# Performance work log

Measured on AMD Instinct MI355X. Metric: run time of the kernel, lower is better.

The kernel has to match this reference:

```python
import jax, jax.numpy as jnp
import numpy as np

B, T, D, H = 64, 1024, 1024, 1024


def setup_inputs() -> dict:
    key = jax.random.key(0)
    k = jax.random.split(key, 5)
    s = 1.0 / np.sqrt(H)  # torch RNNCell init: U(-1/sqrt(H), 1/sqrt(H))
    return {
        "x": jax.random.normal(k[0], (B, T, D), jnp.float32),
        "W_ih": jax.random.uniform(k[1], (H, D), jnp.float32, -s, s),
        "W_hh": jax.random.uniform(k[2], (H, H), jnp.float32, -s, s),
        "b_ih": jax.random.uniform(k[3], (H,), jnp.float32, -s, s),
        "b_hh": jax.random.uniform(k[4], (H,), jnp.float32, -s, s),
    }


def reference(x, W_ih, W_hh, b_ih, b_hh):
    # DelayLineRNN2xOS with a tanh RNNCell:
    #   for i in range(T//2):
    #     h_eve = cell(x[:, 2i],   h_eve); states[:, 2i]   = h_eve
    #     h_odd = cell(x[:, 2i-1], h_odd); states[:, 2i-1] = h_odd   (note 2*0-1 == -1)
    Bn, Tn, _ = x.shape
    Hn = W_hh.shape[0]
    half = Tn // 2

    idx_eve = jnp.arange(half) * 2          # 0, 2, ..., T-2
    idx_odd = (idx_eve - 1) % Tn            # T-1, 1, 3, ..., T-3  (Python neg-index at i=0)

    # Precompute input projections for all timesteps (both biases folded in).
    gi = jnp.einsum('btd,hd->bth', x, W_ih) + b_ih + b_hh  # [B, T, H]
    ge = gi[:, idx_eve].transpose(1, 0, 2)                  # [half, B, H]
    go = gi[:, idx_odd].transpose(1, 0, 2)                  # [half, B, H]

    h0 = jnp.zeros((Bn, Hn), x.dtype)

    def step(carry, inp):
        he, ho = carry
        a, b = inp
        he = jnp.tanh(a + he @ W_hh.T)
        ho = jnp.tanh(b + ho @ W_hh.T)
        return (he, ho), (he, ho)

    (he_f, ho_f), (eve_s, odd_s) = jax.lax.scan(step, (h0, h0), (ge, go))

    # eve_s[i] -> slot 2i ; odd_s[i] -> slot (2i-1) mod T, i.e. sorted odd slots
    # [1, 3, ..., T-1] receive odd_s rolled left by one.
    odd_sorted = jnp.roll(odd_s, -1, axis=0)                # [half, B, H]
    states = jnp.stack([eve_s, odd_sorted], axis=1)         # [half, 2, B, H]
    states = states.reshape(Tn, Bn, Hn).transpose(1, 0, 2)  # [B, T, H]

    return states, he_f[None]  # (states, h_final[1, B, H])
```

## Files before the change

### kernel.cpp

```cpp
#include <hip/hip_runtime.h>

#define B_    64
#define T_    1024
#define H_    1024
#define HALF_ 512
#define NWG_SCAN 128
#define HBUF_HALF 131072

typedef short bf16x8 __attribute__((ext_vector_type(8)));
typedef short bf16x4 __attribute__((ext_vector_type(4)));
typedef _Float16 f16x8 __attribute__((ext_vector_type(8)));
typedef float f32x4  __attribute__((ext_vector_type(4)));
typedef unsigned int u32x4 __attribute__((ext_vector_type(4)));

__device__ __forceinline__ short f2bf(float f) {
    unsigned u = __builtin_bit_cast(unsigned, f);
    u += 0x7fffu + ((u >> 16) & 1u);
    return (short)(u >> 16);
}

__device__ __forceinline__ short f2h(float f) {
    return (short)__builtin_bit_cast(unsigned short, (_Float16)f);
}

__device__ __forceinline__ float tanh_fast(float x) {
    return 1.0f - 2.0f / (__expf(2.0f * x) + 1.0f);
}

__global__ __launch_bounds__(256) void gi_gemm(
        const float* __restrict__ X, const float* __restrict__ Wih,
        const float* __restrict__ bih, const float* __restrict__ bhh,
        float* __restrict__ out) {
    __shared__ short As[128][40];
    __shared__ short Bs[128][40];
    const int bid = blockIdx.x;
    const int tn = bid & 7;
    const int tm = bid >> 3;
    const int tid = threadIdx.x;
    const int l  = tid & 63;
    const int w  = tid >> 6;
    const int wr = w >> 1, wc = w & 1;
    const int lc = l & 15,  lr = l >> 4;

    const float* Ab = X   + (size_t)tm * 128 * 1024;
    const float* Bb = Wih + (size_t)tn * 128 * 1024;
    const int srow = tid >> 3;
    const int sc4  = (tid & 7) * 4;

    f32x4 acc[4][4];
#pragma unroll
    for (int m = 0; m < 4; m++)
#pragma unroll
        for (int n = 0; n < 4; n++) acc[m][n] = (f32x4){0.f, 0.f, 0.f, 0.f};

    f32x4 ra[4], rb[4];
#pragma unroll
    for (int c = 0; c < 4; c++) {
        ra[c] = *reinterpret_cast<const f32x4*>(Ab + (size_t)(srow + 32*c) * 1024 + sc4);
        rb[c] = *reinterpret_cast<const f32x4*>(Bb + (size_t)(srow + 32*c) * 1024 + sc4);
    }

    for (int k0 = 0; k0 < 1024; k0 += 32) {
        __syncthreads();
#pragma unroll
        for (int c = 0; c < 4; c++) {
            bf16x4 va = { f2bf(ra[c].x), f2bf(ra[c].y), f2bf(ra[c].z), f2bf(ra[c].w) };
            bf16x4 vb = { f2bf(rb[c].x), f2bf(rb[c].y), f2bf(rb[c].z), f2bf(rb[c].w) };
            *reinterpret_cast<bf16x4*>(&As[srow + 32*c][sc4]) = va;
            *reinterpret_cast<bf16x4*>(&Bs[srow + 32*c][sc4]) = vb;
        }
        __syncthreads();
        if (k0 + 32 < 1024) {
            const float* Ak = Ab + k0 + 32;
            const float* Bk = Bb + k0 + 32;
#pragma unroll
            for (int c = 0; c < 4; c++) {
                ra[c] = *reinterpret_cast<const f32x4*>(Ak + (size_t)(srow + 32*c) * 1024 + sc4);
                rb[c] = *reinterpret_cast<const f32x4*>(Bk + (size_t)(srow + 32*c) * 1024 + sc4);
            }
        }
        bf16x8 af[4], bfr[4];
#pragma unroll
        for (int m = 0; m < 4; m++)
            af[m] = *reinterpret_cast<bf16x8*>(&As[wr*64 + m*16 + lc][lr*8]);
#pragma unroll
        for (int n = 0; n < 4; n++)
            bfr[n] = *reinterpret_cast<bf16x8*>(&Bs[wc*64 + n*16 + lc][lr*8]);
#pragma unroll
        for (int m = 0; m < 4; m++)
#pragma unroll
            for (int n = 0; n < 4; n++)
                acc[m][n] = __builtin_amdgcn_mfma_f32_16x16x32_bf16(af[m], bfr[n], acc[m][n], 0, 0, 0);
    }

#pragma unroll
    for (int n = 0; n < 4; n++) {
        const int col = tn*128 + wc*64 + n*16 + lc;
        const float bs = bih[col] + bhh[col];
#pragma unroll
        for (int m = 0; m < 4; m++) {
            const int row0 = tm*128 + wr*64 + m*16 + lr*4;
#pragma unroll
            for (int j = 0; j < 4; j++)
                out[(size_t)(row0 + j) * 1024 + col] = acc[m][n][j] + bs;
        }
    }
}

__global__ __launch_bounds__(256, 1) void rnn_scan(
        const float* __restrict__ Whh, float* __restrict__ out,
        short* __restrict__ hbuf) {
    __shared__ short hB[16 * 1024];
    __shared__ short htr[16 * 68];
    const int wg = blockIdx.x;
    const int p  = wg >> 6;
    const int g  = (wg >> 4) & 3;
    const int s  = wg & 15;
    const int tid = threadIdx.x;
    const int l  = tid & 63;
    const int w  = tid >> 6;
    const int lc = l & 15, lr = l >> 4;
    const int sb = tid >> 4;
    const int sg = tid & 15;

    bf16x8 breg[32];
    {
        const float* wrow = Whh + (size_t)(s*64 + w*16 + lc) * 1024;
#pragma unroll
        for (int kc = 0; kc < 32; kc++) {
            f32x4 v0 = *reinterpret_cast<const f32x4*>(wrow + kc*32 + lr*8);
            f32x4 v1 = *reinterpret_cast<const f32x4*>(wrow + kc*32 + lr*8 + 4);
            bf16x8 q = { f2h(v0.x), f2h(v0.y), f2h(v0.z), f2h(v0.w),
                         f2h(v1.x), f2h(v1.y), f2h(v1.z), f2h(v1.w) };
            breg[kc] = q;
        }
    }

    const unsigned hload_base = (unsigned)((p*64 + g*16 + sb) * 1024 + sg*8);
    const unsigned hstore_off = (unsigned)((p*64 + g*16 + sb) * 1024 + s*64 + sg*4);
    const int col = s*64 + w*16 + lc;

    for (int step = 0; step < HALF_; step++) {
        const int tt = (p == 0) ? (2*step) : (step == 0 ? T_-1 : 2*step - 1);
        const int epw = step % 3 + 1;
        const int epv = (step + 2) % 3 + 1;
        f32x4 acc = (f32x4){0.f, 0.f, 0.f, 0.f};
        float gi[4]; unsigned ob[4];

        if (step) {
            bf16x8 hl[8];
            const short* hc = hbuf + (size_t)((step+1) & 1) * HBUF_HALF + hload_base;
#pragma unroll
            for (int c = 0; c < 8; c++)
                asm volatile("global_load_dwordx4 %0, %1, off sc0 sc1"
                             : "=v"(hl[c]) : "v"(hc + c*128) : "memory");
#pragma unroll
            for (int j = 0; j < 4; j++) {
                ob[j] = (unsigned)(((g*16 + lr*4 + j) * T_ + tt) * H_ + col);
                gi[j] = out[ob[j]];
            }
            const unsigned pat = (unsigned)((epv & 1) | (((epv >> 1) & 1) << 16));
            unsigned pend = 0;
            asm volatile("s_waitcnt vmcnt(4)" ::: "memory");
            __builtin_amdgcn_sched_barrier(0);
#pragma unroll
            for (int c = 0; c < 8; c++) {
                u32x4 d = __builtin_bit_cast(u32x4, hl[c]);
                unsigned m = ((d[0] & 0x00010001u) ^ pat) | ((d[1] & 0x00010001u) ^ pat)
                           | ((d[2] & 0x00010001u) ^ pat) | ((d[3] & 0x00010001u) ^ pat);
                if (!__all(m == 0)) pend |= 1u << c;
            }
            while (pend) {
#pragma unroll
                for (int c = 0; c < 8; c++)
                    if (pend & (1u << c))
                        asm volatile("global_load_dwordx4 %0, %1, off sc0 sc1"
                                     : "=v"(hl[c]) : "v"(hc + c*128) : "memory");
                asm volatile("s_waitcnt vmcnt(0)" ::: "memory");
                __builtin_amdgcn_sched_barrier(0);
#pragma unroll
                for (int c = 0; c < 8; c++) {
                    if (pend & (1u << c)) {
                        u32x4 d = __builtin_bit_cast(u32x4, hl[c]);
                        unsigned m = ((d[0] & 0x00010001u) ^ pat) | ((d[1] & 0x00010001u) ^ pat)
                                   | ((d[2] & 0x00010001u) ^ pat) | ((d[3] & 0x00010001u) ^ pat);
                        if (__all(m == 0)) pend &= ~(1u << c);
                    }
                }
            }
#pragma unroll
            for (int c = 0; c < 8; c++) {
                bf16x4 lo = { hl[c][0], hl[c][1], hl[c][2], hl[c][3] };
                bf16x4 hi = { hl[c][4], hl[c][5], hl[c][6], hl[c][7] };
                const int g8 = (sg + c*16) * 2;
                *reinterpret_cast<bf16x4*>(&hB[sb*1024 + (((g8    ) ^ sb) << 2)]) = lo;
                *reinterpret_cast<bf16x4*>(&hB[sb*1024 + (((g8 + 1) ^ sb) << 2)]) = hi;
            }
            __syncthreads();
            f32x4 a0 = (f32x4){0,0,0,0}, a1 = (f32x4){0,0,0,0};
            f32x4 a2 = (f32x4){0,0,0,0}, a3 = (f32x4){0,0,0,0};
#pragma unroll
            for (int kc = 0; kc < 32; kc += 4) {
#pragma unroll
                for (int q = 0; q < 4; q++) {
                    const int k8 = (kc + q) * 8 + lr * 2;
                    bf16x4 lo = *reinterpret_cast<const bf16x4*>(&hB[lc*1024 + (((k8    ) ^ lc) << 2)]);
                    bf16x4 hi = *reinterpret_cast<const bf16x4*>(&hB[lc*1024 + (((k8 + 1) ^ lc) << 2)]);
                    bf16x8 hf = { lo[0], lo[1], lo[2], lo[3], hi[0], hi[1], hi[2], hi[3] };
                    f32x4& aq = (q == 0) ? a0 : (q == 1) ? a1 : (q == 2) ? a2 : a3;
                    aq = __builtin_amdgcn_mfma_f32_16x16x32_f16(
                        __builtin_bit_cast(f16x8, hf),
                        __builtin_bit_cast(f16x8, breg[kc + q]), aq, 0, 0, 0);
                }
            }
            acc = (a0 + a1) + (a2 + a3);
        } else {
#pragma unroll
            for (int j = 0; j < 4; j++) {
                ob[j] = (unsigned)(((g*16 + lr*4 + j) * T_ + tt) * H_ + col);
                gi[j] = out[ob[j]];
            }
        }

        const unsigned short ebit = (unsigned short)((lc & 1) ? ((epw >> 1) & 1) : (epw & 1));
        float hv[4];
#pragma unroll
        for (int j = 0; j < 4; j++) {
            hv[j] = tanh_fast(acc[j] + gi[j]);
            unsigned short u = __builtin_bit_cast(unsigned short, (_Float16)hv[j]);
            u = (unsigned short)((u & 0xFFFEu) | ebit);
            htr[(lr*4 + j)*68 + w*16 + lc] = (short)u;
        }
        __syncthreads();

        if (step < HALF_ - 1) {
            bf16x4 v = *reinterpret_cast<bf16x4*>(&htr[sb*68 + sg*4]);
            short* hn = hbuf + (size_t)(step & 1) * HBUF_HALF + hstore_off;
            asm volatile("global_store_dwordx2 %0, %1, off sc0 sc1"
                         :: "v"(hn), "v"(v) : "memory");
        }

#pragma unroll
        for (int j = 0; j < 4; j++) {
            out[ob[j]] = hv[j];
            if (p == 0 && step == HALF_ - 1)
                out[(unsigned)(B_*T_*H_) + (unsigned)((g*16 + lr*4 + j) * H_ + col)] = hv[j];
        }
    }
}

extern "C" void kernel_launch(void* const* d_in, const int* in_sizes, int n_in,
                              void* d_out, int out_size, void* d_ws, size_t ws_size,
                              hipStream_t stream) {
    const float* X   = (const float*)d_in[0];
    const float* Wih = (const float*)d_in[1];
    const float* Whh = (const float*)d_in[2];
    const float* bih = (const float*)d_in[3];
    const float* bhh = (const float*)d_in[4];
    float* out = (float*)d_out;

    short* hbuf = (short*)d_ws;

    hipMemsetAsync(hbuf, 0, (size_t)2 * HBUF_HALF * 2, stream);
    gi_gemm<<<dim3(4096), dim3(256), 0, stream>>>(X, Wih, bih, bhh, out);
    rnn_scan<<<dim3(NWG_SCAN), dim3(256), 0, stream>>>(Whh, out, hbuf);
}
```

Before: 2.094 ms.

## Remap scan workgroups per XCD and poll hidden state through local L2

New measurement: 4.353 ms. 2.08x slower.

```diff
diff --git a/kernel.cpp b/kernel.cpp
--- a/kernel.cpp
+++ b/kernel.cpp
@@ -6,6 +6,7 @@
 #define HALF_ 512
 #define NWG_SCAN 128
 #define HBUF_HALF 131072
+#define LOCAL_ROUNDS 8
 
 typedef short bf16x8 __attribute__((ext_vector_type(8)));
 typedef short bf16x4 __attribute__((ext_vector_type(4)));
@@ -109,13 +110,13 @@
 
 __global__ __launch_bounds__(256, 1) void rnn_scan(
         const float* __restrict__ Whh, float* __restrict__ out,
-        short* __restrict__ hbuf) {
+        short* __restrict__ hloc, short* __restrict__ hrem) {
     __shared__ short hB[16 * 1024];
     __shared__ short htr[16 * 68];
     const int wg = blockIdx.x;
-    const int p  = wg >> 6;
-    const int g  = (wg >> 4) & 3;
-    const int s  = wg & 15;
+    const int p  = (wg >> 2) & 1;
+    const int g  = wg & 3;
+    const int s  = wg >> 3;
     const int tid = threadIdx.x;
     const int l  = tid & 63;
     const int w  = tid >> 6;
@@ -149,11 +150,13 @@
 
         if (step) {
             bf16x8 hl[8];
-            const short* hc = hbuf + (size_t)((step+1) & 1) * HBUF_HALF + hload_base;
+            const size_t hoff = (size_t)((step+1) & 1) * HBUF_HALF + hload_base;
+            const short* hcl = hloc + hoff;
+            const short* hcr = hrem + hoff;
 #pragma unroll
             for (int c = 0; c < 8; c++)
-                asm volatile("global_load_dwordx4 %0, %1, off sc0 sc1"
-                             : "=v"(hl[c]) : "v"(hc + c*128) : "memory");
+                asm volatile("global_load_dwordx4 %0, %1, off sc0"
+                             : "=v"(hl[c]) : "v"(hcl + c*128) : "memory");
 #pragma unroll
             for (int j = 0; j < 4; j++) {
                 ob[j] = (unsigned)(((g*16 + lr*4 + j) * T_ + tt) * H_ + col);
@@ -170,12 +173,21 @@
                            | ((d[2] & 0x00010001u) ^ pat) | ((d[3] & 0x00010001u) ^ pat);
                 if (!__all(m == 0)) pend |= 1u << c;
             }
+            int rounds = 0;
             while (pend) {
-#pragma unroll
-                for (int c = 0; c < 8; c++)
-                    if (pend & (1u << c))
-                        asm volatile("global_load_dwordx4 %0, %1, off sc0 sc1"
-                                     : "=v"(hl[c]) : "v"(hc + c*128) : "memory");
+                if (rounds < LOCAL_ROUNDS) {
+#pragma unroll
+                    for (int c = 0; c < 8; c++)
+                        if (pend & (1u << c))
+                            asm volatile("global_load_dwordx4 %0, %1, off sc0"
+                                         : "=v"(hl[c]) : "v"(hcl + c*128) : "memory");
+                } else {
+#pragma unroll
+                    for (int c = 0; c < 8; c++)
+                        if (pend & (1u << c))
+                            asm volatile("global_load_dwordx4 %0, %1, off sc0 sc1"
+                                         : "=v"(hl[c]) : "v"(hcr + c*128) : "memory");
+                }
                 asm volatile("s_waitcnt vmcnt(0)" ::: "memory");
                 __builtin_amdgcn_sched_barrier(0);
 #pragma unroll
@@ -187,6 +199,7 @@
                         if (__all(m == 0)) pend &= ~(1u << c);
                     }
                 }
+                rounds++;
             }
 #pragma unroll
             for (int c = 0; c < 8; c++) {
@@ -235,9 +248,13 @@
 
         if (step < HALF_ - 1) {
             bf16x4 v = *reinterpret_cast<bf16x4*>(&htr[sb*68 + sg*4]);
-            short* hn = hbuf + (size_t)(step & 1) * HBUF_HALF + hstore_off;
+            const size_t off = (size_t)(step & 1) * HBUF_HALF + hstore_off;
+            short* hnl = hloc + off;
+            short* hnr = hrem + off;
+            asm volatile("global_store_dwordx2 %0, %1, off sc0"
+                         :: "v"(hnl), "v"(v) : "memory");
             asm volatile("global_store_dwordx2 %0, %1, off sc0 sc1"
-                         :: "v"(hn), "v"(v) : "memory");
+                         :: "v"(hnr), "v"(v) : "memory");
         }
 
 #pragma unroll
@@ -259,9 +276,10 @@
     const float* bhh = (const float*)d_in[4];
     float* out = (float*)d_out;
 
-    short* hbuf = (short*)d_ws;
-
-    hipMemsetAsync(hbuf, 0, (size_t)2 * HBUF_HALF * 2, stream);
+    short* hloc = (short*)d_ws;
+    short* hrem = hloc + 2 * HBUF_HALF;
+
+    hipMemsetAsync(d_ws, 0, (size_t)2 * HBUF_HALF * 2 * 2, stream);
     gi_gemm<<<dim3(4096), dim3(256), 0, stream>>>(X, Wih, bih, bhh, out);
-    rnn_scan<<<dim3(NWG_SCAN), dim3(256), 0, stream>>>(Whh, out, hbuf);
-}
+    rnn_scan<<<dim3(NWG_SCAN), dim3(256), 0, stream>>>(Whh, out, hloc, hrem);
+}
```

## Software-pipeline next-step h and gi loads in RNN scan, vectorize output stores

Applied to the files above, without the earlier changes.

After: 2.287 ms. +9.2%, slower.

```diff
diff --git a/kernel.cpp b/kernel.cpp
--- a/kernel.cpp
+++ b/kernel.cpp
@@ -26,6 +26,14 @@
 __device__ __forceinline__ float tanh_fast(float x) {
     return 1.0f - 2.0f / (__expf(2.0f * x) + 1.0f);
 }
+
+#define BAR() do { \
+    __builtin_amdgcn_sched_barrier(0); \
+    asm volatile("s_waitcnt lgkmcnt(0)" ::: "memory"); \
+    __builtin_amdgcn_sched_barrier(0); \
+    __builtin_amdgcn_s_barrier(); \
+    __builtin_amdgcn_sched_barrier(0); \
+} while (0)
 
 __global__ __launch_bounds__(256) void gi_gemm(
         const float* __restrict__ X, const float* __restrict__ Wih,
@@ -107,11 +115,126 @@
     }
 }
 
+#define STEP_BODY(STEP_, GIC_, GIN_)                                           \
+{                                                                              \
+    const int step = (STEP_);                                                  \
+    const int epw = step % 3 + 1;                                              \
+    const int epv = (step + 2) % 3 + 1;                                        \
+    f32x4 acc;                                                                 \
+    if (step) {                                                                \
+        asm volatile("s_waitcnt vmcnt(2)" ::: "memory");                       \
+        __builtin_amdgcn_sched_barrier(0);                                     \
+        const unsigned pat = (unsigned)((epv & 1) | (((epv >> 1) & 1) << 16)); \
+        unsigned pend = 0;                                                     \
+        _Pragma("unroll")                                                      \
+        for (int c = 0; c < 8; c++) {                                          \
+            u32x4 d = __builtin_bit_cast(u32x4, hl[c]);                        \
+            unsigned m = ((d[0] & 0x00010001u) ^ pat) | ((d[1] & 0x00010001u) ^ pat)  \
+                       | ((d[2] & 0x00010001u) ^ pat) | ((d[3] & 0x00010001u) ^ pat); \
+            if (!__all(m == 0)) pend |= 1u << c;                               \
+        }                                                                      \
+        const short* hc = hbuf + (size_t)((step+1) & 1) * HBUF_HALF + hload_base; \
+        while (pend) {                                                         \
+            _Pragma("unroll")                                                  \
+            for (int c = 0; c < 8; c++)                                        \
+                if (pend & (1u << c))                                          \
+                    asm volatile("global_load_dwordx4 %0, %1, off sc0 sc1"     \
+                                 : "=v"(hl[c]) : "v"(hc + c*128) : "memory");  \
+            asm volatile("s_waitcnt vmcnt(0)" ::: "memory");                   \
+            __builtin_amdgcn_sched_barrier(0);                                 \
+            _Pragma("unroll")                                                  \
+            for (int c = 0; c < 8; c++) {                                      \
+                if (pend & (1u << c)) {                                        \
+                    u32x4 d = __builtin_bit_cast(u32x4, hl[c]);                \
+                    unsigned m = ((d[0] & 0x00010001u) ^ pat) | ((d[1] & 0x00010001u) ^ pat)  \
+                               | ((d[2] & 0x00010001u) ^ pat) | ((d[3] & 0x00010001u) ^ pat); \
+                    if (__all(m == 0)) pend &= ~(1u << c);                     \
+                }                                                              \
+            }                                                                  \
+        }                                                                      \
+        _Pragma("unroll")                                                      \
+        for (int c = 0; c < 8; c++) {                                          \
+            bf16x4 lo = { hl[c][0], hl[c][1], hl[c][2], hl[c][3] };            \
+            bf16x4 hi = { hl[c][4], hl[c][5], hl[c][6], hl[c][7] };            \
+            const int g8 = (sg + c*16) * 2;                                    \
+            *reinterpret_cast<bf16x4*>(&hB[sb*1024 + (((g8    ) ^ sb) << 2)]) = lo; \
+            *reinterpret_cast<bf16x4*>(&hB[sb*1024 + (((g8 + 1) ^ sb) << 2)]) = hi; \
+        }                                                                      \
+        BAR();                                                                 \
+        f32x4 a0 = (f32x4){0,0,0,0}, a1 = (f32x4){0,0,0,0};                    \
+        f32x4 a2 = (f32x4){0,0,0,0}, a3 = (f32x4){0,0,0,0};                    \
+        _Pragma("unroll")                                                      \
+        for (int kc = 0; kc < 32; kc += 4) {                                   \
+            _Pragma("unroll")                                                  \
+            for (int q = 0; q < 4; q++) {                                      \
+                const int k8 = (kc + q) * 8 + lr * 2;                          \
+                bf16x4 lo = *reinterpret_cast<const bf16x4*>(&hB[lc*1024 + (((k8    ) ^ lc) << 2)]); \
+                bf16x4 hi = *reinterpret_cast<const bf16x4*>(&hB[lc*1024 + (((k8 + 1) ^ lc) << 2)]); \
+                bf16x8 hf = { lo[0], lo[1], lo[2], lo[3], hi[0], hi[1], hi[2], hi[3] }; \
+                f32x4& aq = (q == 0) ? a0 : (q == 1) ? a1 : (q == 2) ? a2 : a3; \
+                aq = __builtin_amdgcn_mfma_f32_16x16x32_f16(                   \
+                    __builtin_bit_cast(f16x8, hf),                             \
+                    __builtin_bit_cast(f16x8, breg[kc + q]), aq, 0, 0, 0);     \
+            }                                                                  \
+        }                                                                      \
+        acc = (a0 + a1) + (a2 + a3);                                           \
+    } else {                                                                   \
+        asm volatile("s_waitcnt vmcnt(0)" ::: "memory");                       \
+        __builtin_amdgcn_sched_barrier(0);                                     \
+        acc = (f32x4){0.f, 0.f, 0.f, 0.f};                                     \
+    }                                                                          \
+                       \
+    if (step + 1 < HALF_) {                                                    \
+        const int t2 = (p == 0) ? (2*(step+1)) : (2*(step+1) - 1);             \
+        _Pragma("unroll")                                                      \
+        for (int j = 0; j < 4; j++) {                                          \
+            const float* ga = out + (size_t)(((g*16 + lr*4 + j) * T_ + t2) * H_ + col); \
+            asm volatile("global_load_dword %0, %1, off"                       \
+                         : "=v"(GIN_[j]) : "v"(ga) : "memory");                \
+        }                                                                      \
+        const short* hc2 = hbuf + (size_t)(step & 1) * HBUF_HALF + hload_base; \
+        _Pragma("unroll")                                                      \
+        for (int c = 0; c < 8; c++)                                            \
+            asm volatile("global_load_dwordx4 %0, %1, off sc0 sc1"             \
+                         : "=v"(hl[c]) : "v"(hc2 + c*128) : "memory");         \
+    }                                                                          \
+                 \
+    const int tt = (p == 0) ? (2*step) : (step == 0 ? T_-1 : 2*step - 1);      \
+    const unsigned short ebit = (unsigned short)((lc & 1) ? ((epw >> 1) & 1) : (epw & 1)); \
+    _Pragma("unroll")                                                          \
+    for (int j = 0; j < 4; j++) {                                              \
+        float hv = tanh_fast(acc[j] + GIC_[j]);                                \
+        unsigned short u = __builtin_bit_cast(unsigned short, (_Float16)hv);   \
+        u = (unsigned short)((u & 0xFFFEu) | ebit);                            \
+        htr [(lr*4 + j)*68 + w*16 + lc] = (short)u;                            \
+        htrF[(lr*4 + j)*68 + w*16 + lc] = hv;                                  \
+    }                                                                          \
+    BAR();                                                                     \
+    if (step < HALF_ - 1) {                                                    \
+        bf16x4 v = *reinterpret_cast<bf16x4*>(&htr[sb*68 + sg*4]);             \
+        short* hn = hbuf + (size_t)(step & 1) * HBUF_HALF + hstore_off;        \
+        asm volatile("global_store_dwordx2 %0, %1, off sc0 sc1"                \
+                     :: "v"(hn), "v"(v) : "memory");                           \
+    }                                                                          \
+    {                                                                          \
+        f32x4 ov = *reinterpret_cast<f32x4*>(&htrF[sb*68 + sg*4]);             \
+        float* op_ = out + (size_t)(((g*16 + sb) * T_ + tt) * H_ + s*64 + sg*4); \
+        asm volatile("global_store_dwordx4 %0, %1, off"                        \
+                     :: "v"(op_), "v"(ov) : "memory");                         \
+        if (p == 0 && step == HALF_ - 1) {                                     \
+            float* fp_ = out + (size_t)B_*T_*H_ + (size_t)((g*16 + sb) * H_ + s*64 + sg*4); \
+            asm volatile("global_store_dwordx4 %0, %1, off"                    \
+                         :: "v"(fp_), "v"(ov) : "memory");                     \
+        }                                                                      \
+    }                                                                          \
+}
+
 __global__ __launch_bounds__(256, 1) void rnn_scan(
         const float* __restrict__ Whh, float* __restrict__ out,
         short* __restrict__ hbuf) {
     __shared__ short hB[16 * 1024];
     __shared__ short htr[16 * 68];
+    __shared__ float htrF[16 * 68];
     const int wg = blockIdx.x;
     const int p  = wg >> 6;
     const int g  = (wg >> 4) & 3;
@@ -140,112 +263,22 @@
     const unsigned hstore_off = (unsigned)((p*64 + g*16 + sb) * 1024 + s*64 + sg*4);
     const int col = s*64 + w*16 + lc;
 
-    for (int step = 0; step < HALF_; step++) {
-        const int tt = (p == 0) ? (2*step) : (step == 0 ? T_-1 : 2*step - 1);
-        const int epw = step % 3 + 1;
-        const int epv = (step + 2) % 3 + 1;
-        f32x4 acc = (f32x4){0.f, 0.f, 0.f, 0.f};
-        float gi[4]; unsigned ob[4];
-
-        if (step) {
-            bf16x8 hl[8];
-            const short* hc = hbuf + (size_t)((step+1) & 1) * HBUF_HALF + hload_base;
-#pragma unroll
-            for (int c = 0; c < 8; c++)
-                asm volatile("global_load_dwordx4 %0, %1, off sc0 sc1"
-                             : "=v"(hl[c]) : "v"(hc + c*128) : "memory");
-#pragma unroll
-            for (int j = 0; j < 4; j++) {
-                ob[j] = (unsigned)(((g*16 + lr*4 + j) * T_ + tt) * H_ + col);
-                gi[j] = out[ob[j]];
-            }
-            const unsigned pat = (unsigned)((epv & 1) | (((epv >> 1) & 1) << 16));
-            unsigned pend = 0;
-            asm volatile("s_waitcnt vmcnt(4)" ::: "memory");
-            __builtin_amdgcn_sched_barrier(0);
-#pragma unroll
-            for (int c = 0; c < 8; c++) {
-                u32x4 d = __builtin_bit_cast(u32x4, hl[c]);
-                unsigned m = ((d[0] & 0x00010001u) ^ pat) | ((d[1] & 0x00010001u) ^ pat)
-                           | ((d[2] & 0x00010001u) ^ pat) | ((d[3] & 0x00010001u) ^ pat);
-                if (!__all(m == 0)) pend |= 1u << c;
-            }
-            while (pend) {
-#pragma unroll
-                for (int c = 0; c < 8; c++)
-                    if (pend & (1u << c))
-                        asm volatile("global_load_dwordx4 %0, %1, off sc0 sc1"
-                                     : "=v"(hl[c]) : "v"(hc + c*128) : "memory");
-                asm volatile("s_waitcnt vmcnt(0)" ::: "memory");
-                __builtin_amdgcn_sched_barrier(0);
-#pragma unroll
-                for (int c = 0; c < 8; c++) {
-                    if (pend & (1u << c)) {
-                        u32x4 d = __builtin_bit_cast(u32x4, hl[c]);
-                        unsigned m = ((d[0] & 0x00010001u) ^ pat) | ((d[1] & 0x00010001u) ^ pat)
-                                   | ((d[2] & 0x00010001u) ^ pat) | ((d[3] & 0x00010001u) ^ pat);
-                        if (__all(m == 0)) pend &= ~(1u << c);
-                    }
-                }
-            }
-#pragma unroll
-            for (int c = 0; c < 8; c++) {
-                bf16x4 lo = { hl[c][0], hl[c][1], hl[c][2], hl[c][3] };
-                bf16x4 hi = { hl[c][4], hl[c][5], hl[c][6], hl[c][7] };
-                const int g8 = (sg + c*16) * 2;
-                *reinterpret_cast<bf16x4*>(&hB[sb*1024 + (((g8    ) ^ sb) << 2)]) = lo;
-                *reinterpret_cast<bf16x4*>(&hB[sb*1024 + (((g8 + 1) ^ sb) << 2)]) = hi;
-            }
-            __syncthreads();
-            f32x4 a0 = (f32x4){0,0,0,0}, a1 = (f32x4){0,0,0,0};
-            f32x4 a2 = (f32x4){0,0,0,0}, a3 = (f32x4){0,0,0,0};
-#pragma unroll
-            for (int kc = 0; kc < 32; kc += 4) {
-#pragma unroll
-                for (int q = 0; q < 4; q++) {
-                    const int k8 = (kc + q) * 8 + lr * 2;
-                    bf16x4 lo = *reinterpret_cast<const bf16x4*>(&hB[lc*1024 + (((k8    ) ^ lc) << 2)]);
-                    bf16x4 hi = *reinterpret_cast<const bf16x4*>(&hB[lc*1024 + (((k8 + 1) ^ lc) << 2)]);
-                    bf16x8 hf = { lo[0], lo[1], lo[2], lo[3], hi[0], hi[1], hi[2], hi[3] };
-                    f32x4& aq = (q == 0) ? a0 : (q == 1) ? a1 : (q == 2) ? a2 : a3;
-                    aq = __builtin_amdgcn_mfma_f32_16x16x32_f16(
-                        __builtin_bit_cast(f16x8, hf),
-                        __builtin_bit_cast(f16x8, breg[kc + q]), aq, 0, 0, 0);
-                }
-            }
-            acc = (a0 + a1) + (a2 + a3);
-        } else {
-#pragma unroll
-            for (int j = 0; j < 4; j++) {
-                ob[j] = (unsigned)(((g*16 + lr*4 + j) * T_ + tt) * H_ + col);
-                gi[j] = out[ob[j]];
-            }
-        }
-
-        const unsigned short ebit = (unsigned short)((lc & 1) ? ((epw >> 1) & 1) : (epw & 1));
-        float hv[4];
+    bf16x8 hl[8];
+    float giA[4], giB[4];
+
+    {
+        const int t0 = (p == 0) ? 0 : T_ - 1;
 #pragma unroll
         for (int j = 0; j < 4; j++) {
-            hv[j] = tanh_fast(acc[j] + gi[j]);
-            unsigned short u = __builtin_bit_cast(unsigned short, (_Float16)hv[j]);
-            u = (unsigned short)((u & 0xFFFEu) | ebit);
-            htr[(lr*4 + j)*68 + w*16 + lc] = (short)u;
-        }
-        __syncthreads();
-
-        if (step < HALF_ - 1) {
-            bf16x4 v = *reinterpret_cast<bf16x4*>(&htr[sb*68 + sg*4]);
-            short* hn = hbuf + (size_t)(step & 1) * HBUF_HALF + hstore_off;
-            asm volatile("global_store_dwordx2 %0, %1, off sc0 sc1"
-                         :: "v"(hn), "v"(v) : "memory");
-        }
-
-#pragma unroll
-        for (int j = 0; j < 4; j++) {
-            out[ob[j]] = hv[j];
-            if (p == 0 && step == HALF_ - 1)
-                out[(unsigned)(B_*T_*H_) + (unsigned)((g*16 + lr*4 + j) * H_ + col)] = hv[j];
-        }
+            const float* ga = out + (size_t)(((g*16 + lr*4 + j) * T_ + t0) * H_ + col);
+            asm volatile("global_load_dword %0, %1, off"
+                         : "=v"(giA[j]) : "v"(ga) : "memory");
+        }
+    }
+
+    for (int sp = 0; sp < HALF_; sp += 2) {
+        STEP_BODY(sp,     giA, giB)
+        STEP_BODY(sp + 1, giB, giA)
     }
 }
 
```
